# Optimization experiments

Hardware: AMD Instinct MI355X
Metric: run time of the kernel (lower is better)

The kernel has to match this reference:

```python
import jax, jax.numpy as jnp
import numpy as np

EMB = 1024
NHEAD = 16
HEAD_DIM = EMB // NHEAD  # 64
L = 2048
NEG = -1e30


def setup_inputs() -> dict:
    key = jax.random.key(0)
    ks = jax.random.split(key, 8)
    # xavier_uniform bound for square [EMB, EMB] matrices
    bound = float(np.sqrt(6.0 / (EMB + EMB)))
    def xavier(k):
        return jax.random.uniform(k, (EMB, EMB), jnp.float32, -bound, bound)
    return {
        "q": jax.random.normal(ks[0], (L, EMB), jnp.float32),
        "k": jax.random.normal(ks[1], (L, EMB), jnp.float32),
        "v": jax.random.normal(ks[2], (L, EMB), jnp.float32),
        "mask": jax.random.randint(ks[3], (NHEAD, L, L), 0, 2) > 0,
        "Wq": xavier(ks[4]),
        "Wk": xavier(ks[5]),
        "Wv": xavier(ks[6]),
        "Wo": xavier(ks[7]),
    }


def reference(q, k, v, mask, Wq, Wk, Wv, Wo):
    scaling = HEAD_DIM ** -0.5
    # F.linear(x, W) = x @ W.T ; reshape to [H, L, D]
    Q = (q @ Wq.T).reshape(L, NHEAD, HEAD_DIM).swapaxes(0, 1)
    K = (k @ Wk.T).reshape(L, NHEAD, HEAD_DIM).swapaxes(0, 1)
    V = (v @ Wv.T).reshape(L, NHEAD, HEAD_DIM).swapaxes(0, 1)
    scores = jnp.einsum("hld,hmd->hlm", Q, K) * scaling  # [H, L, L]
    scores = jnp.where(mask, jnp.asarray(NEG, scores.dtype), scores)
    p = jax.nn.softmax(scores, axis=-1)
    # attn_mask=True: multiplicative re-mask after softmax (custom path)
    p = p * (~mask).astype(p.dtype)
    # dropout is a no-op in eval mode
    attn_out = jnp.einsum("hlm,hmd->hld", p, V)  # [H, L, D]
    attn_out = attn_out.swapaxes(0, 1).reshape(L, EMB)
    return attn_out @ Wo.T
```

## Files before the change

### kernel.cpp

```cpp
#include <hip/hip_runtime.h>
#include <stdint.h>

#define EMB   1024
#define NHEAD 16
#define HDIM  64
#define SEQ   2048

typedef unsigned short ushort_t;
typedef unsigned int   uint32;
typedef __attribute__((ext_vector_type(8))) short bfrag;
typedef __attribute__((ext_vector_type(4))) float ffrag;

#define MFMA(a, b, c) __builtin_amdgcn_mfma_f32_16x16x32_bf16((a), (b), (c), 0, 0, 0)

__device__ inline ushort_t f2bf(float f) {
  uint32 u = __float_as_uint(f);
  u += 0x7FFFu + ((u >> 16) & 1u);
  return (ushort_t)(u >> 16);
}
__device__ inline uint32 pack2(float a, float b) {
  return (uint32)f2bf(a) | ((uint32)f2bf(b) << 16);
}

__device__ inline void glds16(const ushort_t* g, ushort_t* l) {
  __builtin_amdgcn_global_load_lds(
      (const __attribute__((address_space(1))) uint32*)(uintptr_t)g,
      (__attribute__((address_space(3))) uint32*)(uintptr_t)l, 16, 0, 0);
}

__global__ void detect_mask_kernel(const uint32* __restrict__ mw, int* __restrict__ flag) {
  uint32 w = mw[threadIdx.x];
  bool is4 = (w == 0u) || (w == 1u) || (w == 0x3F800000u);
  unsigned long long bad = __ballot(!is4);
  if (threadIdx.x == 0) flag[0] = (bad == 0ull) ? 1 : 0;
}

__global__ __launch_bounds__(256) void prep(
    const void* __restrict__ maskp, const int* __restrict__ flag, ushort_t* __restrict__ bmout,
    const float4* __restrict__ q,  const float4* __restrict__ k,  const float4* __restrict__ v,
    const float4* __restrict__ wq, const float4* __restrict__ wk, const float4* __restrict__ wv,
    const float4* __restrict__ wo,
    uint2* __restrict__ qb,  uint2* __restrict__ kb,  uint2* __restrict__ vb,
    uint2* __restrict__ wqb, uint2* __restrict__ wkb, uint2* __restrict__ wvb,
    uint2* __restrict__ wob)
{
  const int tid = threadIdx.x;
  int b = blockIdx.x;
  if (b < 16384) {
    size_t t = (size_t)b * 256 + tid;
    size_t row = t >> 7;
    int c16 = (int)(t & 127);
    size_t base = row * SEQ + (size_t)c16 * 16;
    ushort_t mv = 0;
    if (*flag) {
      const uint4* p = (const uint4*)((const uint32*)maskp + base);
      uint4 a0 = p[0], a1 = p[1], a2 = p[2], a3 = p[3];
      uint32 aw[16] = {a0.x,a0.y,a0.z,a0.w, a1.x,a1.y,a1.z,a1.w,
                       a2.x,a2.y,a2.z,a2.w, a3.x,a3.y,a3.z,a3.w};
      #pragma unroll
      for (int i = 0; i < 16; ++i) mv |= (ushort_t)((aw[i] != 0u) ? 1u : 0u) << i;
    } else {
      uint4 b0 = *(const uint4*)((const unsigned char*)maskp + base);
      uint32 bw[4] = {b0.x, b0.y, b0.z, b0.w};
      #pragma unroll
      for (int i = 0; i < 16; ++i)
        mv |= (ushort_t)((((bw[i >> 2] >> ((i & 3) * 8)) & 0xFFu) != 0u) ? 1u : 0u) << i;
    }
    bmout[t] = mv;
    return;
  }
  b -= 16384;
  const float4* src; uint2* dst; int t;
  if (b < 6144) {
    int s = b >> 11; t = (b & 2047) * 256 + tid;
    src = (s == 0) ? q  : (s == 1) ? k  : v;
    dst = (s == 0) ? qb : (s == 1) ? kb : vb;
  } else {
    int s = (b - 6144) >> 10; t = ((b - 6144) & 1023) * 256 + tid;
    src = (s == 0) ? wq  : (s == 1) ? wk  : (s == 2) ? wv  : wo;
    dst = (s == 0) ? wqb : (s == 1) ? wkb : (s == 2) ? wvb : wob;
  }
  float4 f = src[t];
  uint2 o; o.x = pack2(f.x, f.y); o.y = pack2(f.z, f.w);
  dst[t] = o;
}

template<int MODE, int BN>
__device__ inline void gemm_body(const ushort_t* A, const ushort_t* B, void* Cp,
                                 int m0, int n0, ushort_t* As, ushort_t* Bs) {
  const int tid = threadIdx.x, lane = tid & 63, w = tid >> 6;
  const int wm = (w >> 1) * 64, wn = (w & 1) * (BN / 2);
  const int col = lane & 15, g = lane >> 4;
  constexpr int TN = BN / 32;
  constexpr int BIT = BN / 32;

  ffrag acc[4][TN] = {};

  for (int k0 = 0; k0 < EMB; k0 += 64) {
    __syncthreads();
    #pragma unroll
    for (int it = 0; it < 4; ++it) {
      int p = it * 256 + tid;
      int row = p >> 3, pc = p & 7;
      glds16(A + (size_t)(m0 + row) * EMB + k0 + (pc ^ (row & 7)) * 8, &As[p * 8]);
    }
    #pragma unroll
    for (int it = 0; it < BIT; ++it) {
      int p = it * 256 + tid;
      int row = p >> 3, pc = p & 7;
      glds16(B + (size_t)(n0 + row) * EMB + k0 + (pc ^ (row & 7)) * 8, &Bs[p * 8]);
    }
    __syncthreads();

    #pragma unroll
    for (int c = 0; c < 2; ++c) {
      bfrag av[4], bv[TN];
      #pragma unroll
      for (int t = 0; t < 4; ++t) {
        int ra = wm + t * 16 + col;
        av[t] = *(const bfrag*)&As[ra * 64 + ((c * 4 + g) ^ (ra & 7)) * 8];
      }
      #pragma unroll
      for (int t = 0; t < TN; ++t) {
        int rb = wn + t * 16 + col;
        bv[t] = *(const bfrag*)&Bs[rb * 64 + ((c * 4 + g) ^ (rb & 7)) * 8];
      }
      #pragma unroll
      for (int tm = 0; tm < 4; ++tm)
        #pragma unroll
        for (int tn = 0; tn < TN; ++tn)
          acc[tm][tn] = MFMA(av[tm], bv[tn], acc[tm][tn]);
    }
  }

  const int rbase = g * 4;
  #pragma unroll
  for (int tm = 0; tm < 4; ++tm)
    #pragma unroll
    for (int tn = 0; tn < TN; ++tn)
      #pragma unroll
      for (int r = 0; r < 4; ++r) {
        int m = m0 + wm + tm * 16 + rbase + r;
        int n = n0 + wn + tn * 16 + col;
        float vv = acc[tm][tn][r];
        if (MODE == 0) {
          ((ushort_t*)Cp)[((size_t)(n >> 6) * SEQ + m) * HDIM + (n & 63)] = f2bf(vv);
        } else if (MODE == 1) {
          ((ushort_t*)Cp)[((size_t)(m >> 6) * HDIM + (m & 63)) * SEQ + n] = f2bf(vv);
        } else {
          ((float*)Cp)[(size_t)m * EMB + n] = vv;
        }
      }
}

__global__ __launch_bounds__(256) void gemm_qkv(
    const ushort_t* __restrict__ qb, const ushort_t* __restrict__ kb, const ushort_t* __restrict__ vb,
    const ushort_t* __restrict__ Wqb, const ushort_t* __restrict__ Wkb, const ushort_t* __restrict__ Wvb,
    ushort_t* __restrict__ Qb, ushort_t* __restrict__ Kb, ushort_t* __restrict__ Vtb)
{
  __shared__ ushort_t As[128 * 64];
  __shared__ ushort_t Bs[128 * 64];
  const int z = blockIdx.y, bid = blockIdx.x;
  if (z == 0) {
    gemm_body<0, 128>(qb, Wqb, Qb, (bid >> 3) * 128, (bid & 7) * 128, As, Bs);
  } else if (z == 1) {
    gemm_body<0, 128>(kb, Wkb, Kb, (bid >> 3) * 128, (bid & 7) * 128, As, Bs);
  } else {
    gemm_body<1, 128>(Wvb, vb, Vtb, (bid >> 4) * 128, (bid & 15) * 128, As, Bs);
  }
}

__global__ __launch_bounds__(256) void gemm_out(
    const ushort_t* __restrict__ A, const ushort_t* __restrict__ B, float* __restrict__ C)
{
  __shared__ ushort_t As[128 * 64];
  __shared__ ushort_t Bs[128 * 64];
  gemm_body<2, 128>(A, B, (void*)C, blockIdx.y * 128, blockIdx.x * 128, As, Bs);
}

__global__ __launch_bounds__(256) void attn_mfma(
    const ushort_t* __restrict__ Qb,
    const ushort_t* __restrict__ Kb,
    const ushort_t* __restrict__ Vtb,
    const ushort_t* __restrict__ bm,
    ushort_t* __restrict__ attnb)
{
  __shared__ ushort_t KVs[2][2][64 * 64];
  __shared__ ushort_t Ps[4][16 * 72];

  const int tid  = threadIdx.x;
  const int lane = tid & 63;
  const int w    = tid >> 6;
  const int h    = blockIdx.y;
  const int l0   = blockIdx.x * 64;
  const int col  = lane & 15, g = lane >> 4, kg8 = g * 8, rbase = g * 4;

  ushort_t* pw = &Ps[w][0];

  {
    int rl = lane >> 2, seg = (lane & 3) * 16;
    const uint4* pq = (const uint4*)(Qb + ((size_t)h * SEQ + l0 + w * 16 + rl) * HDIM + seg);
    uint4 q0 = pq[0], q1 = pq[1];
    *(uint4*)&pw[rl * 72 + seg] = q0;
    *(uint4*)&pw[rl * 72 + seg + 8] = q1;
  }
  bfrag qf[2];
  qf[0] = *(const bfrag*)&pw[col * 72 + kg8];
  qf[1] = *(const bfrag*)&pw[col * 72 + 32 + kg8];

  auto stage_kv = [&](int kt_, int buf) {
    #pragma unroll
    for (int it = 0; it < 2; ++it) {
      int p = it * 256 + tid;
      int row = p >> 3, pc = p & 7;
      int sc = (pc ^ (row & 7)) * 8;
      glds16(Kb + ((size_t)h * SEQ + kt_ + row) * HDIM + sc, &KVs[buf][0][p * 8]);
      glds16(Vtb + ((size_t)h * HDIM + row) * SEQ + kt_ + sc, &KVs[buf][1][p * 8]);
    }
  };
  stage_kv(0, 0);

  const size_t bmbase = ((size_t)h * SEQ + l0 + w * 16 + col) * 128 + g;
  ushort_t mv_next = bm[bmbase];

  float lsum = 0.f;
  ffrag oacc[4] = {};

  for (int t = 0; t < 32; ++t) {
    const int buf = t & 1;
    __syncthreads();
    stage_kv(((t + 1) & 31) * 64, buf ^ 1);

    const ushort_t* Kc = &KVs[buf][0][0];
    const ushort_t* Vc = &KVs[buf][1][0];

    int mvi = (int)mv_next;
    mv_next = bm[bmbase + (size_t)((t + 1) & 31) * 4];

    ffrag s[4] = {};
    #pragma unroll
    for (int c = 0; c < 2; ++c)
      #pragma unroll
      for (int tn = 0; tn < 4; ++tn) {
        int row = tn * 16 + col;
        bfrag kf = *(const bfrag*)&Kc[row * 64 + ((c * 4 + g) ^ (row & 7)) * 8];
        s[tn] = MFMA(kf, qf[c], s[tn]);
      }

    #pragma unroll
    for (int tn = 0; tn < 4; ++tn) {
      int m16 = __shfl(mvi, tn * 16 + col, 64);
      float p0, p1, p2, p3;
      {
        bool k0m = ((m16 >> (rbase + 0)) & 1) != 0;
        bool k1m = ((m16 >> (rbase + 1)) & 1) != 0;
        bool k2m = ((m16 >> (rbase + 2)) & 1) != 0;
        bool k3m = ((m16 >> (rbase + 3)) & 1) != 0;
        p0 = k0m ? 0.f : __expf(s[tn][0] * 0.125f);
        p1 = k1m ? 0.f : __expf(s[tn][1] * 0.125f);
        p2 = k2m ? 0.f : __expf(s[tn][2] * 0.125f);
        p3 = k3m ? 0.f : __expf(s[tn][3] * 0.125f);
      }
      lsum += (p0 + p1) + (p2 + p3);
      uint2 pk; pk.x = pack2(p0, p1); pk.y = pack2(p2, p3);
      *(uint2*)&pw[col * 72 + tn * 16 + rbase] = pk;
    }

    #pragma unroll
    for (int c = 0; c < 2; ++c) {
      bfrag af = *(const bfrag*)&pw[col * 72 + c * 32 + kg8];
      #pragma unroll
      for (int tn = 0; tn < 4; ++tn) {
        int row = tn * 16 + col;
        bfrag vf = *(const bfrag*)&Vc[row * 64 + ((c * 4 + g) ^ (row & 7)) * 8];
        oacc[tn] = MFMA(af, vf, oacc[tn]);
      }
    }
  }

  float s_ = lsum;
  s_ += __shfl_xor(s_, 16, 64);
  s_ += __shfl_xor(s_, 32, 64);
  float invf = (s_ > 0.f) ? (1.0f / s_) : 0.0f;
  float inv[4];
  #pragma unroll
  for (int r = 0; r < 4; ++r) inv[r] = __shfl(invf, rbase + r, 64);

  #pragma unroll
  for (int tn = 0; tn < 4; ++tn)
    #pragma unroll
    for (int r = 0; r < 4; ++r) {
      int qg = l0 + w * 16 + rbase + r;
      attnb[(size_t)qg * EMB + h * HDIM + tn * 16 + col] = f2bf(oacc[tn][r] * inv[r]);
    }
}

extern "C" void kernel_launch(void* const* d_in, const int* in_sizes, int n_in,
                              void* d_out, int out_size, void* d_ws, size_t ws_size,
                              hipStream_t stream) {
  const float* q    = (const float*)d_in[0];
  const float* k    = (const float*)d_in[1];
  const float* v    = (const float*)d_in[2];
  const void*  mask =               d_in[3];
  const float* Wq   = (const float*)d_in[4];
  const float* Wk   = (const float*)d_in[5];
  const float* Wv   = (const float*)d_in[6];
  const float* Wo   = (const float*)d_in[7];

  char* ws = (char*)d_ws;
  const size_t MB = 1024 * 1024;
  ushort_t* qb    = (ushort_t*)(ws);
  ushort_t* kb    = (ushort_t*)(ws + 4  * MB);
  ushort_t* vb    = (ushort_t*)(ws + 8  * MB);
  ushort_t* Wqb   = (ushort_t*)(ws + 12 * MB);
  ushort_t* Wkb   = (ushort_t*)(ws + 14 * MB);
  ushort_t* Wvb   = (ushort_t*)(ws + 16 * MB);
  ushort_t* Wob   = (ushort_t*)(ws + 18 * MB);
  ushort_t* Qb    = (ushort_t*)(ws + 20 * MB);
  ushort_t* Kb    = (ushort_t*)(ws + 24 * MB);
  ushort_t* Vtb   = (ushort_t*)(ws + 28 * MB);
  int*      flag  = (int*)     (ws + 32 * MB);
  ushort_t* bmask = (ushort_t*)(ws + 33 * MB);
  ushort_t* attnb = qb;

  detect_mask_kernel<<<1, 64, 0, stream>>>((const uint32*)mask, flag);

  prep<<<26624, 256, 0, stream>>>(
      mask, flag, bmask,
      (const float4*)q, (const float4*)k, (const float4*)v,
      (const float4*)Wq, (const float4*)Wk, (const float4*)Wv, (const float4*)Wo,
      (uint2*)qb, (uint2*)kb, (uint2*)vb,
      (uint2*)Wqb, (uint2*)Wkb, (uint2*)Wvb, (uint2*)Wob);

  gemm_qkv<<<dim3(128, 3), 256, 0, stream>>>(qb, kb, vb, Wqb, Wkb, Wvb, Qb, Kb, Vtb);

  attn_mfma<<<dim3(SEQ / 64, NHEAD), 256, 0, stream>>>(Qb, Kb, Vtb, bmask, attnb);

  gemm_out<<<dim3(8, 16), 256, 0, stream>>>(attnb, Wob, (float*)d_out);
}
```

Measured before the change: 499.5 us.

## Fuse all stages into one cooperative persistent kernel with grid syncs

Replaces the five separate launches (mask detect, prep, QKV GEMM, attention, output GEMM) with one cooperative kernel of 768 blocks that runs each stage in turn, separated by grid-wide syncs. GEMM N-tiles shrink from 128 to 64, so the QKV and output GEMMs launch more blocks and fill the grid. This removes per-launch overhead and inter-kernel gaps. In exchange it adds grid barrier costs, grid-stride loops in the prep stage, and fewer idle blocks available for latency hiding. The old multi-kernel path is kept as a fallback if the cooperative launch fails.

Result: slower. 769.7 us (+54.1%).

```diff
diff --git a/kernel.cpp b/kernel.cpp
--- a/kernel.cpp
+++ b/kernel.cpp
@@ -1,10 +1,14 @@
 #include <hip/hip_runtime.h>
+#include <hip/hip_cooperative_groups.h>
 #include <stdint.h>
 
 #define EMB   1024
 #define NHEAD 16
 #define HDIM  64
 #define SEQ   2048
+#define FGRID 768
+
+namespace cg = cooperative_groups;
 
 typedef unsigned short ushort_t;
 typedef unsigned int   uint32;
@@ -26,6 +30,271 @@
   __builtin_amdgcn_global_load_lds(
       (const __attribute__((address_space(1))) uint32*)(uintptr_t)g,
       (__attribute__((address_space(3))) uint32*)(uintptr_t)l, 16, 0, 0);
+}
+
+template<int MODE, int BN>
+__device__ inline void gemm_body(const ushort_t* A, const ushort_t* B, void* Cp,
+                                 int m0, int n0, ushort_t* As, ushort_t* Bs) {
+  const int tid = threadIdx.x, lane = tid & 63, w = tid >> 6;
+  const int wm = (w >> 1) * 64, wn = (w & 1) * (BN / 2);
+  const int col = lane & 15, g = lane >> 4;
+  constexpr int TN = BN / 32;
+  constexpr int BIT = BN / 32;
+
+  ffrag acc[4][TN] = {};
+
+  for (int k0 = 0; k0 < EMB; k0 += 64) {
+    __syncthreads();
+    #pragma unroll
+    for (int it = 0; it < 4; ++it) {
+      int p = it * 256 + tid;
+      int row = p >> 3, pc = p & 7;
+      glds16(A + (size_t)(m0 + row) * EMB + k0 + (pc ^ (row & 7)) * 8, &As[p * 8]);
+    }
+    #pragma unroll
+    for (int it = 0; it < BIT; ++it) {
+      int p = it * 256 + tid;
+      int row = p >> 3, pc = p & 7;
+      glds16(B + (size_t)(n0 + row) * EMB + k0 + (pc ^ (row & 7)) * 8, &Bs[p * 8]);
+    }
+    __syncthreads();
+
+    #pragma unroll
+    for (int c = 0; c < 2; ++c) {
+      bfrag av[4], bv[TN];
+      #pragma unroll
+      for (int t = 0; t < 4; ++t) {
+        int ra = wm + t * 16 + col;
+        av[t] = *(const bfrag*)&As[ra * 64 + ((c * 4 + g) ^ (ra & 7)) * 8];
+      }
+      #pragma unroll
+      for (int t = 0; t < TN; ++t) {
+        int rb = wn + t * 16 + col;
+        bv[t] = *(const bfrag*)&Bs[rb * 64 + ((c * 4 + g) ^ (rb & 7)) * 8];
+      }
+      #pragma unroll
+      for (int tm = 0; tm < 4; ++tm)
+        #pragma unroll
+        for (int tn = 0; tn < TN; ++tn)
+          acc[tm][tn] = MFMA(av[tm], bv[tn], acc[tm][tn]);
+    }
+  }
+
+  const int rbase = g * 4;
+  #pragma unroll
+  for (int tm = 0; tm < 4; ++tm)
+    #pragma unroll
+    for (int tn = 0; tn < TN; ++tn)
+      #pragma unroll
+      for (int r = 0; r < 4; ++r) {
+        int m = m0 + wm + tm * 16 + rbase + r;
+        int n = n0 + wn + tn * 16 + col;
+        float vv = acc[tm][tn][r];
+        if (MODE == 0) {
+          ((ushort_t*)Cp)[((size_t)(n >> 6) * SEQ + m) * HDIM + (n & 63)] = f2bf(vv);
+        } else if (MODE == 1) {
+          ((ushort_t*)Cp)[((size_t)(m >> 6) * HDIM + (m & 63)) * SEQ + n] = f2bf(vv);
+        } else {
+          ((float*)Cp)[(size_t)m * EMB + n] = vv;
+        }
+      }
+}
+
+__global__ __launch_bounds__(256, 3) void fused(
+    const float* __restrict__ q,  const float* __restrict__ k,  const float* __restrict__ v,
+    const void*  __restrict__ maskp,
+    const float* __restrict__ Wq, const float* __restrict__ Wk, const float* __restrict__ Wv,
+    const float* __restrict__ Wo,
+    ushort_t* __restrict__ qb,  ushort_t* __restrict__ kb,  ushort_t* __restrict__ vb,
+    ushort_t* __restrict__ Wqb, ushort_t* __restrict__ Wkb, ushort_t* __restrict__ Wvb,
+    ushort_t* __restrict__ Wob,
+    ushort_t* __restrict__ Qb,  ushort_t* __restrict__ Kb,  ushort_t* __restrict__ Vtb,
+    ushort_t* __restrict__ bm,  float* __restrict__ out)
+{
+  __shared__ __align__(16) ushort_t smem[20992];
+
+  cg::grid_group grid = cg::this_grid();
+
+  const int tid  = threadIdx.x;
+  const int lane = tid & 63;
+  const int w    = tid >> 6;
+
+  {
+    uint32 mw = ((const uint32*)maskp)[lane];
+    bool is4 = (mw == 0u) || (mw == 1u) || (mw == 0x3F800000u);
+    const bool flag4 = (__ballot(!is4) == 0ull);
+
+    const int gtid    = blockIdx.x * 256 + tid;
+    const int gstride = FGRID * 256;
+
+    for (int t = gtid; t < NHEAD * SEQ * 128; t += gstride) {
+      size_t row = (size_t)(t >> 7);
+      int c16 = t & 127;
+      size_t base = row * SEQ + (size_t)c16 * 16;
+      ushort_t mv = 0;
+      if (flag4) {
+        const uint4* p = (const uint4*)((const uint32*)maskp + base);
+        uint4 a0 = p[0], a1 = p[1], a2 = p[2], a3 = p[3];
+        uint32 aw[16] = {a0.x,a0.y,a0.z,a0.w, a1.x,a1.y,a1.z,a1.w,
+                         a2.x,a2.y,a2.z,a2.w, a3.x,a3.y,a3.z,a3.w};
+        #pragma unroll
+        for (int i = 0; i < 16; ++i) mv |= (ushort_t)((aw[i] != 0u) ? 1u : 0u) << i;
+      } else {
+        uint4 b0 = *(const uint4*)((const unsigned char*)maskp + base);
+        uint32 bw[4] = {b0.x, b0.y, b0.z, b0.w};
+        #pragma unroll
+        for (int i = 0; i < 16; ++i)
+          mv |= (ushort_t)((((bw[i >> 2] >> ((i & 3) * 8)) & 0xFFu) != 0u) ? 1u : 0u) << i;
+      }
+      bm[t] = mv;
+    }
+
+    auto cvt = [&](const float* src, ushort_t* dst, int n4) {
+      const float4* s4 = (const float4*)src;
+      uint2* d2 = (uint2*)dst;
+      for (int t = gtid; t < n4; t += gstride) {
+        float4 f = s4[t];
+        uint2 o; o.x = pack2(f.x, f.y); o.y = pack2(f.z, f.w);
+        d2[t] = o;
+      }
+    };
+    cvt(q,  qb,  SEQ * EMB / 4);
+    cvt(k,  kb,  SEQ * EMB / 4);
+    cvt(v,  vb,  SEQ * EMB / 4);
+    cvt(Wq, Wqb, EMB * EMB / 4);
+    cvt(Wk, Wkb, EMB * EMB / 4);
+    cvt(Wv, Wvb, EMB * EMB / 4);
+    cvt(Wo, Wob, EMB * EMB / 4);
+  }
+
+  grid.sync();
+
+  {
+    ushort_t* As = smem;
+    ushort_t* Bs = smem + 128 * 64;
+    int j = blockIdx.x, z = j >> 8, bid = j & 255;
+    if (z == 0) {
+      gemm_body<0, 64>(qb, Wqb, Qb, (bid >> 4) * 128, (bid & 15) * 64, As, Bs);
+    } else if (z == 1) {
+      gemm_body<0, 64>(kb, Wkb, Kb, (bid >> 4) * 128, (bid & 15) * 64, As, Bs);
+    } else {
+      gemm_body<1, 64>(Wvb, vb, Vtb, (bid >> 5) * 128, (bid & 31) * 64, As, Bs);
+    }
+  }
+
+  grid.sync();
+
+  if (blockIdx.x < (SEQ / 64) * NHEAD) {
+    const int h    = blockIdx.x >> 5;
+    const int l0   = (blockIdx.x & 31) * 64;
+    const int col  = lane & 15, g = lane >> 4, kg8 = g * 8, rbase = g * 4;
+
+    ushort_t* KV = smem;
+    ushort_t* pw = smem + 16384 + w * 1152;
+    ushort_t* attnb = qb;
+
+    {
+      int rl = lane >> 2, seg = (lane & 3) * 16;
+      const uint4* pq = (const uint4*)(Qb + ((size_t)h * SEQ + l0 + w * 16 + rl) * HDIM + seg);
+      uint4 q0 = pq[0], q1 = pq[1];
+      *(uint4*)&pw[rl * 72 + seg] = q0;
+      *(uint4*)&pw[rl * 72 + seg + 8] = q1;
+    }
+    bfrag qf[2];
+    qf[0] = *(const bfrag*)&pw[col * 72 + kg8];
+    qf[1] = *(const bfrag*)&pw[col * 72 + 32 + kg8];
+
+    auto stage_kv = [&](int kt_, int buf) {
+      #pragma unroll
+      for (int it = 0; it < 2; ++it) {
+        int p = it * 256 + tid;
+        int row = p >> 3, pc = p & 7;
+        int sc = (pc ^ (row & 7)) * 8;
+        glds16(Kb  + ((size_t)h * SEQ + kt_ + row) * HDIM + sc, &KV[(buf * 2 + 0) * 4096 + p * 8]);
+        glds16(Vtb + ((size_t)h * HDIM + row) * SEQ + kt_ + sc, &KV[(buf * 2 + 1) * 4096 + p * 8]);
+      }
+    };
+    stage_kv(0, 0);
+
+    const size_t bmbase = ((size_t)h * SEQ + l0 + w * 16 + col) * 128 + g;
+    ushort_t mv_next = bm[bmbase];
+
+    float lsum = 0.f;
+    ffrag oacc[4] = {};
+
+    for (int t = 0; t < 32; ++t) {
+      const int buf = t & 1;
+      __syncthreads();
+      stage_kv(((t + 1) & 31) * 64, buf ^ 1);
+
+      const ushort_t* Kc = &KV[(buf * 2 + 0) * 4096];
+      const ushort_t* Vc = &KV[(buf * 2 + 1) * 4096];
+
+      int mvi = (int)mv_next;
+      mv_next = bm[bmbase + (size_t)((t + 1) & 31) * 4];
+
+      ffrag s[4] = {};
+      #pragma unroll
+      for (int c = 0; c < 2; ++c)
+        #pragma unroll
+        for (int tn = 0; tn < 4; ++tn) {
+          int row = tn * 16 + col;
+          bfrag kf = *(const bfrag*)&Kc[row * 64 + ((c * 4 + g) ^ (row & 7)) * 8];
+          s[tn] = MFMA(kf, qf[c], s[tn]);
+        }
+
+      #pragma unroll
+      for (int tn = 0; tn < 4; ++tn) {
+        int m16 = __shfl(mvi, tn * 16 + col, 64);
+        bool k0m = ((m16 >> (rbase + 0)) & 1) != 0;
+        bool k1m = ((m16 >> (rbase + 1)) & 1) != 0;
+        bool k2m = ((m16 >> (rbase + 2)) & 1) != 0;
+        bool k3m = ((m16 >> (rbase + 3)) & 1) != 0;
+        float p0 = k0m ? 0.f : __expf(s[tn][0] * 0.125f);
+        float p1 = k1m ? 0.f : __expf(s[tn][1] * 0.125f);
+        float p2 = k2m ? 0.f : __expf(s[tn][2] * 0.125f);
+        float p3 = k3m ? 0.f : __expf(s[tn][3] * 0.125f);
+        lsum += (p0 + p1) + (p2 + p3);
+        uint2 pk; pk.x = pack2(p0, p1); pk.y = pack2(p2, p3);
+        *(uint2*)&pw[col * 72 + tn * 16 + rbase] = pk;
+      }
+
+      #pragma unroll
+      for (int c = 0; c < 2; ++c) {
+        bfrag af = *(const bfrag*)&pw[col * 72 + c * 32 + kg8];
+        #pragma unroll
+        for (int tn = 0; tn < 4; ++tn) {
+          int row = tn * 16 + col;
+          bfrag vf = *(const bfrag*)&Vc[row * 64 + ((c * 4 + g) ^ (row & 7)) * 8];
+          oacc[tn] = MFMA(af, vf, oacc[tn]);
+        }
+      }
+    }
+
+    float s_ = lsum;
+    s_ += __shfl_xor(s_, 16, 64);
+    s_ += __shfl_xor(s_, 32, 64);
+    float invf = (s_ > 0.f) ? (1.0f / s_) : 0.0f;
+    float inv[4];
+    #pragma unroll
+    for (int r = 0; r < 4; ++r) inv[r] = __shfl(invf, rbase + r, 64);
+
+    #pragma unroll
+    for (int tn = 0; tn < 4; ++tn)
+      #pragma unroll
+      for (int r = 0; r < 4; ++r) {
+        int qg = l0 + w * 16 + rbase + r;
+        attnb[(size_t)qg * EMB + h * HDIM + tn * 16 + col] = f2bf(oacc[tn][r] * inv[r]);
+      }
+  }
+
+  grid.sync();
+
+  if (blockIdx.x < 256) {
+    int j = blockIdx.x;
+    gemm_body<2, 64>(qb , Wob, (void*)out, (j >> 4) * 128, (j & 15) * 64,
+                     smem, smem + 128 * 64);
+  }
 }
 
 __global__ void detect_mask_kernel(const uint32* __restrict__ mw, int* __restrict__ flag) {
@@ -35,7 +304,7 @@
   if (threadIdx.x == 0) flag[0] = (bad == 0ull) ? 1 : 0;
 }
 
-__global__ __launch_bounds__(256) void prep(
+__global__ __launch_bounds__(256) void prep_k(
     const void* __restrict__ maskp, const int* __restrict__ flag, ushort_t* __restrict__ bmout,
     const float4* __restrict__ q,  const float4* __restrict__ k,  const float4* __restrict__ v,
     const float4* __restrict__ wq, const float4* __restrict__ wk, const float4* __restrict__ wv,
@@ -85,104 +354,34 @@
   dst[t] = o;
 }
 
-template<int MODE, int BN>
-__device__ inline void gemm_body(const ushort_t* A, const ushort_t* B, void* Cp,
-                                 int m0, int n0, ushort_t* As, ushort_t* Bs) {
-  const int tid = threadIdx.x, lane = tid & 63, w = tid >> 6;
-  const int wm = (w >> 1) * 64, wn = (w & 1) * (BN / 2);
-  const int col = lane & 15, g = lane >> 4;
-  constexpr int TN = BN / 32;
-  constexpr int BIT = BN / 32;
-
-  ffrag acc[4][TN] = {};
-
-  for (int k0 = 0; k0 < EMB; k0 += 64) {
-    __syncthreads();
-    #pragma unroll
-    for (int it = 0; it < 4; ++it) {
-      int p = it * 256 + tid;
-      int row = p >> 3, pc = p & 7;
-      glds16(A + (size_t)(m0 + row) * EMB + k0 + (pc ^ (row & 7)) * 8, &As[p * 8]);
-    }
-    #pragma unroll
-    for (int it = 0; it < BIT; ++it) {
-      int p = it * 256 + tid;
-      int row = p >> 3, pc = p & 7;
-      glds16(B + (size_t)(n0 + row) * EMB + k0 + (pc ^ (row & 7)) * 8, &Bs[p * 8]);
-    }
-    __syncthreads();
-
-    #pragma unroll
-    for (int c = 0; c < 2; ++c) {
-      bfrag av[4], bv[TN];
-      #pragma unroll
-      for (int t = 0; t < 4; ++t) {
-        int ra = wm + t * 16 + col;
-        av[t] = *(const bfrag*)&As[ra * 64 + ((c * 4 + g) ^ (ra & 7)) * 8];
-      }
-      #pragma unroll
-      for (int t = 0; t < TN; ++t) {
-        int rb = wn + t * 16 + col;
-        bv[t] = *(const bfrag*)&Bs[rb * 64 + ((c * 4 + g) ^ (rb & 7)) * 8];
-      }
-      #pragma unroll
-      for (int tm = 0; tm < 4; ++tm)
-        #pragma unroll
-        for (int tn = 0; tn < TN; ++tn)
-          acc[tm][tn] = MFMA(av[tm], bv[tn], acc[tm][tn]);
-    }
-  }
-
-  const int rbase = g * 4;
-  #pragma unroll
-  for (int tm = 0; tm < 4; ++tm)
-    #pragma unroll
-    for (int tn = 0; tn < TN; ++tn)
-      #pragma unroll
-      for (int r = 0; r < 4; ++r) {
-        int m = m0 + wm + tm * 16 + rbase + r;
-        int n = n0 + wn + tn * 16 + col;
-        float vv = acc[tm][tn][r];
-        if (MODE == 0) {
-          ((ushort_t*)Cp)[((size_t)(n >> 6) * SEQ + m) * HDIM + (n & 63)] = f2bf(vv);
-        } else if (MODE == 1) {
-          ((ushort_t*)Cp)[((size_t)(m >> 6) * HDIM + (m & 63)) * SEQ + n] = f2bf(vv);
-        } else {
-          ((float*)Cp)[(size_t)m * EMB + n] = vv;
-        }
-      }
-}
-
-__global__ __launch_bounds__(256) void gemm_qkv(
+__global__ __launch_bounds__(256) void gemm_qkv_k(
     const ushort_t* __restrict__ qb, const ushort_t* __restrict__ kb, const ushort_t* __restrict__ vb,
     const ushort_t* __restrict__ Wqb, const ushort_t* __restrict__ Wkb, const ushort_t* __restrict__ Wvb,
     ushort_t* __restrict__ Qb, ushort_t* __restrict__ Kb, ushort_t* __restrict__ Vtb)
 {
   __shared__ ushort_t As[128 * 64];
-  __shared__ ushort_t Bs[128 * 64];
+  __shared__ ushort_t Bs[64 * 64];
   const int z = blockIdx.y, bid = blockIdx.x;
   if (z == 0) {
-    gemm_body<0, 128>(qb, Wqb, Qb, (bid >> 3) * 128, (bid & 7) * 128, As, Bs);
+    gemm_body<0, 64>(qb, Wqb, Qb, (bid >> 4) * 128, (bid & 15) * 64, As, Bs);
   } else if (z == 1) {
-    gemm_body<0, 128>(kb, Wkb, Kb, (bid >> 3) * 128, (bid & 7) * 128, As, Bs);
+    gemm_body<0, 64>(kb, Wkb, Kb, (bid >> 4) * 128, (bid & 15) * 64, As, Bs);
   } else {
-    gemm_body<1, 128>(Wvb, vb, Vtb, (bid >> 4) * 128, (bid & 15) * 128, As, Bs);
-  }
-}
-
-__global__ __launch_bounds__(256) void gemm_out(
+    gemm_body<1, 64>(Wvb, vb, Vtb, (bid >> 5) * 128, (bid & 31) * 64, As, Bs);
+  }
+}
+
+__global__ __launch_bounds__(256) void gemm_out_k(
     const ushort_t* __restrict__ A, const ushort_t* __restrict__ B, float* __restrict__ C)
 {
   __shared__ ushort_t As[128 * 64];
-  __shared__ ushort_t Bs[128 * 64];
-  gemm_body<2, 128>(A, B, (void*)C, blockIdx.y * 128, blockIdx.x * 128, As, Bs);
-}
-
-__global__ __launch_bounds__(256) void attn_mfma(
-    const ushort_t* __restrict__ Qb,
-    const ushort_t* __restrict__ Kb,
-    const ushort_t* __restrict__ Vtb,
-    const ushort_t* __restrict__ bm,
+  __shared__ ushort_t Bs[64 * 64];
+  gemm_body<2, 64>(A, B, (void*)C, blockIdx.y * 128, blockIdx.x * 64, As, Bs);
+}
+
+__global__ __launch_bounds__(256) void attn_mfma_k(
+    const ushort_t* __restrict__ Qb, const ushort_t* __restrict__ Kb,
+    const ushort_t* __restrict__ Vtb, const ushort_t* __restrict__ bm,
     ushort_t* __restrict__ attnb)
 {
   __shared__ ushort_t KVs[2][2][64 * 64];
@@ -196,7 +395,6 @@
   const int col  = lane & 15, g = lane >> 4, kg8 = g * 8, rbase = g * 4;
 
   ushort_t* pw = &Ps[w][0];
-
   {
     int rl = lane >> 2, seg = (lane & 3) * 16;
     const uint4* pq = (const uint4*)(Qb + ((size_t)h * SEQ + l0 + w * 16 + rl) * HDIM + seg);
@@ -250,17 +448,14 @@
     #pragma unroll
     for (int tn = 0; tn < 4; ++tn) {
       int m16 = __shfl(mvi, tn * 16 + col, 64);
-      float p0, p1, p2, p3;
-      {
-        bool k0m = ((m16 >> (rbase + 0)) & 1) != 0;
-        bool k1m = ((m16 >> (rbase + 1)) & 1) != 0;
-        bool k2m = ((m16 >> (rbase + 2)) & 1) != 0;
-        bool k3m = ((m16 >> (rbase + 3)) & 1) != 0;
-        p0 = k0m ? 0.f : __expf(s[tn][0] * 0.125f);
-        p1 = k1m ? 0.f : __expf(s[tn][1] * 0.125f);
-        p2 = k2m ? 0.f : __expf(s[tn][2] * 0.125f);
-        p3 = k3m ? 0.f : __expf(s[tn][3] * 0.125f);
-      }
+      bool k0m = ((m16 >> (rbase + 0)) & 1) != 0;
+      bool k1m = ((m16 >> (rbase + 1)) & 1) != 0;
+      bool k2m = ((m16 >> (rbase + 2)) & 1) != 0;
+      bool k3m = ((m16 >> (rbase + 3)) & 1) != 0;
+      float p0 = k0m ? 0.f : __expf(s[tn][0] * 0.125f);
+      float p1 = k1m ? 0.f : __expf(s[tn][1] * 0.125f);
+      float p2 = k2m ? 0.f : __expf(s[tn][2] * 0.125f);
+      float p3 = k3m ? 0.f : __expf(s[tn][3] * 0.125f);
       lsum += (p0 + p1) + (p2 + p3);
       uint2 pk; pk.x = pack2(p0, p1); pk.y = pack2(p2, p3);
       *(uint2*)&pw[col * 72 + tn * 16 + rbase] = pk;
@@ -321,20 +516,28 @@
   ushort_t* Vtb   = (ushort_t*)(ws + 28 * MB);
   int*      flag  = (int*)     (ws + 32 * MB);
   ushort_t* bmask = (ushort_t*)(ws + 33 * MB);
-  ushort_t* attnb = qb;
-
-  detect_mask_kernel<<<1, 64, 0, stream>>>((const uint32*)mask, flag);
-
-  prep<<<26624, 256, 0, stream>>>(
-      mask, flag, bmask,
-      (const float4*)q, (const float4*)k, (const float4*)v,
-      (const float4*)Wq, (const float4*)Wk, (const float4*)Wv, (const float4*)Wo,
-      (uint2*)qb, (uint2*)kb, (uint2*)vb,
-      (uint2*)Wqb, (uint2*)Wkb, (uint2*)Wvb, (uint2*)Wob);
-
-  gemm_qkv<<<dim3(128, 3), 256, 0, stream>>>(qb, kb, vb, Wqb, Wkb, Wvb, Qb, Kb, Vtb);
-
-  attn_mfma<<<dim3(SEQ / 64, NHEAD), 256, 0, stream>>>(Qb, Kb, Vtb, bmask, attnb);
-
-  gemm_out<<<dim3(8, 16), 256, 0, stream>>>(attnb, Wob, (float*)d_out);
-}
+  float*    outp  = (float*)d_out;
+
+  void* params[20] = {
+    (void*)&q, (void*)&k, (void*)&v, (void*)&mask,
+    (void*)&Wq, (void*)&Wk, (void*)&Wv, (void*)&Wo,
+    (void*)&qb, (void*)&kb, (void*)&vb,
+    (void*)&Wqb, (void*)&Wkb, (void*)&Wvb, (void*)&Wob,
+    (void*)&Qb, (void*)&Kb, (void*)&Vtb, (void*)&bmask, (void*)&outp
+  };
+
+  hipError_t e = hipLaunchCooperativeKernel((void*)fused, dim3(FGRID), dim3(256),
+                                            params, 0, stream);
+  if (e != hipSuccess) {
+    detect_mask_kernel<<<1, 64, 0, stream>>>((const uint32*)mask, flag);
+    prep_k<<<26624, 256, 0, stream>>>(
+        mask, flag, bmask,
+        (const float4*)q, (const float4*)k, (const float4*)v,
+        (const float4*)Wq, (const float4*)Wk, (const float4*)Wv, (const float4*)Wo,
+        (uint2*)qb, (uint2*)kb, (uint2*)vb,
+        (uint2*)Wqb, (uint2*)Wkb, (uint2*)Wvb, (uint2*)Wob);
+    gemm_qkv_k<<<dim3(256, 3), 256, 0, stream>>>(qb, kb, vb, Wqb, Wkb, Wvb, Qb, Kb, Vtb);
+    attn_mfma_k<<<dim3(SEQ / 64, NHEAD), 256, 0, stream>>>(Qb, Kb, Vtb, bmask, qb);
+    gemm_out_k<<<dim3(16, 16), 256, 0, stream>>>(qb, Wob, outp);
+  }
+}
```
